# Performance work log

Measured on AMD Instinct MI355X. Metric: run time of the kernel, lower is better.

## Reference

```python
import jax, jax.numpy as jnp
import numpy as np

N, E = 50000, 800000
H, C = 4, 32          # heads, per-head channels
IN_DIM = 128
NEG_SLOPE = 0.2


def gat_conv(x, edge_index, W, a_src, a_dst, b):
    """PyG-style GATConv: Wx, per-edge leaky-relu logits, dst-segment softmax,
    scatter-weighted aggregation, concat heads, add bias. Self-loops added."""
    n = x.shape[0]
    loops = jnp.arange(n, dtype=edge_index.dtype)
    src = jnp.concatenate([edge_index[0], loops])
    dst = jnp.concatenate([edge_index[1], loops])
    xw = (x @ W).reshape(n, H, C)                      # [N,H,C]
    alpha_src = jnp.sum(xw * a_src, axis=-1)           # [N,H]
    alpha_dst = jnp.sum(xw * a_dst, axis=-1)           # [N,H]
    e = jax.nn.leaky_relu(alpha_src[src] + alpha_dst[dst], NEG_SLOPE)  # [E+N,H]
    m = jax.ops.segment_max(e, dst, num_segments=n)    # stable softmax per dst
    e = jnp.exp(e - m[dst])
    denom = jax.ops.segment_sum(e, dst, num_segments=n)
    alpha = e / denom[dst]                             # [E+N,H]
    out = jax.ops.segment_sum(alpha[:, :, None] * xw[src], dst, num_segments=n)
    return out.reshape(n, H * C) + b


def setup_inputs() -> dict:
    key = jax.random.key(0)
    ks = jax.random.split(key, 12)
    HC = H * C
    x = jax.random.normal(ks[0], (N, IN_DIM), dtype=jnp.float32)
    edge_index = jax.random.randint(ks[1], (2, E), 0, N, dtype=jnp.int32)
    s0 = 1.0 / np.sqrt(IN_DIM)
    s1 = 1.0 / np.sqrt(HC)
    return {
        "x": x,
        "edge_index": edge_index,
        "W0": jax.random.normal(ks[2], (IN_DIM, HC), dtype=jnp.float32) * s0,
        "a_src0": jax.random.normal(ks[3], (H, C), dtype=jnp.float32) * s1,
        "a_dst0": jax.random.normal(ks[4], (H, C), dtype=jnp.float32) * s1,
        "b0": jnp.zeros((HC,), dtype=jnp.float32),
        "W1": jax.random.normal(ks[5], (HC, HC), dtype=jnp.float32) * s1,
        "a_src1": jax.random.normal(ks[6], (H, C), dtype=jnp.float32) * s1,
        "a_dst1": jax.random.normal(ks[7], (H, C), dtype=jnp.float32) * s1,
        "b1": jnp.zeros((HC,), dtype=jnp.float32),
        "Wr": jax.random.normal(ks[8], (HC, 1), dtype=jnp.float32) * s1,
        "br": jnp.zeros((1,), dtype=jnp.float32),
    }


def reference(x, edge_index, W0, a_src0, a_dst0, b0, W1, a_src1, a_dst1, b1, Wr, br):
    h = jax.nn.elu(gat_conv(x, edge_index, W0, a_src0, a_dst0, b0))
    # F.dropout(training=False) -> identity (eval mode)
    h = jax.nn.elu(gat_conv(h, edge_index, W1, a_src1, a_dst1, b1))
    return h @ Wr + br
```

## Files before the change

### kernel.cpp

```cpp
#include <hip/hip_runtime.h>
#include <hip/hip_bf16.h>
#include <hip/hip_fp16.h>

#define DEV __device__ __forceinline__

DEV float lrelu(float x) { return x > 0.f ? x : 0.2f * x; }
DEV float elu(float x)   { return x > 0.f ? x : __expf(x) - 1.f; }

typedef _Float16 v2h __attribute__((ext_vector_type(2)));
DEV float fdot2(__half2 a, __half2 b, float c) {
    union { __half2 h; v2h v; } ua, ub;
    ua.h = a; ub.h = b;
    return __builtin_amdgcn_fdot2(ua.v, ub.v, c, false);
}

#define CAP 64

__global__ __launch_bounds__(256, 8)
void gemm0_scatter(const float* __restrict__ X, const float* __restrict__ W,
                   const float* __restrict__ a_src, const float* __restrict__ a_dst,
                   __half2* __restrict__ xw2, float* __restrict__ asrc,
                   float* __restrict__ adst, int n, int gblk,
                   const int* __restrict__ ei, int* __restrict__ deg,
                   int* __restrict__ col2, int E, int sblk) {
    if ((int)blockIdx.x >= gblk) {
        int stride = sblk * 256;
        for (int e = ((int)blockIdx.x - gblk) * 256 + (int)threadIdx.x; e < E;
             e += stride) {
            int s = ei[e], d = ei[E + e];
            int pos = atomicAdd(&deg[d], 1);
            if (pos < CAP) col2[d * CAP + pos] = s;
        }
        return;
    }
    __shared__ __half2 Xs2[16][68];
    __shared__ __half2 Ws2[16][132];
    int t = threadIdx.x;
    int n0 = (int)blockIdx.x * 64;
    int rg = t >> 4;
    int cg = t & 15;
    int q0 = cg * 8 + ((cg >= 8) ? 4 : 0);

    float acc[4][8];
#pragma unroll
    for (int r = 0; r < 4; ++r)
#pragma unroll
        for (int c = 0; c < 8; ++c) acc[r][c] = 0.f;

    float4 px[2], pw[4];
    auto load_x = [&](int k0, float4* p) {
#pragma unroll
        for (int it = 0; it < 2; ++it) {
            int idx = t + it * 256;
            int row = idx >> 3, kq = idx & 7;
            int gr = n0 + row;
            p[it] = (gr < n) ? *(const float4*)&X[(size_t)gr * 128 + k0 + kq * 4]
                             : make_float4(0.f, 0.f, 0.f, 0.f);
        }
    };
    auto load_w = [&](int k0, float4* p) {
#pragma unroll
        for (int it = 0; it < 2; ++it) {
            int idx = t + it * 256;
            int k2 = idx >> 5, cq = idx & 31;
            p[2 * it]     = *(const float4*)&W[(size_t)(k0 + 2 * k2) * 128 + cq * 4];
            p[2 * it + 1] = *(const float4*)&W[(size_t)(k0 + 2 * k2 + 1) * 128 + cq * 4];
        }
    };
    auto store_lds = [&](const float4* pX, const float4* pW) {
#pragma unroll
        for (int it = 0; it < 2; ++it) {
            int idx = t + it * 256;
            int row = idx >> 3, kq = idx & 7;
            Xs2[kq * 2 + 0][row] = __floats2half2_rn(pX[it].x, pX[it].y);
            Xs2[kq * 2 + 1][row] = __floats2half2_rn(pX[it].z, pX[it].w);
        }
#pragma unroll
        for (int it = 0; it < 2; ++it) {
            int idx = t + it * 256;
            int k2 = idx >> 5, cq = idx & 31;
            const float4 w0 = pW[2 * it], w1 = pW[2 * it + 1];
            union { __half2 h[4]; float4 f; } u;
            u.h[0] = __floats2half2_rn(w0.x, w1.x);
            u.h[1] = __floats2half2_rn(w0.y, w1.y);
            u.h[2] = __floats2half2_rn(w0.z, w1.z);
            u.h[3] = __floats2half2_rn(w0.w, w1.w);
            *(float4*)&Ws2[k2][cq * 4 + ((cq >= 16) ? 4 : 0)] = u.f;
        }
    };

    load_x(0, px);
    load_w(0, pw);
    for (int c4 = 0; c4 < 4; ++c4) {
        store_lds(px, pw);
        __syncthreads();
        if (c4 < 3) { load_x((c4 + 1) * 32, px); load_w((c4 + 1) * 32, pw); }
#pragma unroll 4
        for (int k2 = 0; k2 < 16; ++k2) {
            union { float4 f; __half2 h[4]; } ux, uw0, uw1;
            ux.f  = *(const float4*)&Xs2[k2][rg * 4];
            uw0.f = *(const float4*)&Ws2[k2][q0];
            uw1.f = *(const float4*)&Ws2[k2][q0 + 4];
            __half2 wr[8] = {uw0.h[0], uw0.h[1], uw0.h[2], uw0.h[3],
                             uw1.h[0], uw1.h[1], uw1.h[2], uw1.h[3]};
#pragma unroll
            for (int r = 0; r < 4; ++r)
#pragma unroll
                for (int c = 0; c < 8; ++c)
                    acc[r][c] = fdot2(ux.h[r], wr[c], acc[r][c]);
        }
        __syncthreads();
    }

    int c0 = cg * 8;
    int h = cg >> 2;
    float as8[8], ad8[8];
#pragma unroll
    for (int c = 0; c < 8; ++c) { as8[c] = a_src[c0 + c]; ad8[c] = a_dst[c0 + c]; }
#pragma unroll
    for (int r = 0; r < 4; ++r) {
        int gr = n0 + rg * 4 + r;
        float s_ = 0.f, d_ = 0.f;
#pragma unroll
        for (int c = 0; c < 8; ++c) {
            s_ = fmaf(acc[r][c], as8[c], s_);
            d_ = fmaf(acc[r][c], ad8[c], d_);
        }
        s_ += __shfl_xor(s_, 1); s_ += __shfl_xor(s_, 2);
        d_ += __shfl_xor(d_, 1); d_ += __shfl_xor(d_, 2);
        if (gr < n) {
            __half2* rowp = &xw2[(size_t)gr * 64 + (c0 >> 1)];
            rowp[0] = __floats2half2_rn(acc[r][0], acc[r][1]);
            rowp[1] = __floats2half2_rn(acc[r][2], acc[r][3]);
            rowp[2] = __floats2half2_rn(acc[r][4], acc[r][5]);
            rowp[3] = __floats2half2_rn(acc[r][6], acc[r][7]);
            if ((t & 3) == 0) { asrc[gr * 4 + h] = s_; adst[gr * 4 + h] = d_; }
        }
    }
}

__global__ __launch_bounds__(512, 8)
void agg0_gemm1(const __half2* __restrict__ xw2a, const float* __restrict__ asrc0,
                const float* __restrict__ adst0, const int* __restrict__ col2,
                const int* __restrict__ deg, const float* __restrict__ bias,
                const float* __restrict__ W, const float* __restrict__ a_src,
                const float* __restrict__ a_dst, __half2* __restrict__ xw2b,
                float* __restrict__ asrc1, float* __restrict__ adst1, int n) {
    __shared__ __half2 Xh2[64][66];
    __shared__ __half2 Ws2[16][132];
    int t = threadIdx.x;
    int n0 = (int)blockIdx.x * 64;
    int l = t & 63;
    int q = t >> 6;

    float4 pw[2];
    auto load_w = [&](int k0) {
        int k2 = t >> 5, cq = t & 31;
        pw[0] = *(const float4*)&W[(size_t)(k0 + 2 * k2) * 128 + cq * 4];
        pw[1] = *(const float4*)&W[(size_t)(k0 + 2 * k2 + 1) * 128 + cq * 4];
    };
    auto store_w = [&]() {
        int k2 = t >> 5, cq = t & 31;
        union { __half2 h[4]; float4 f; } u;
        u.h[0] = __floats2half2_rn(pw[0].x, pw[1].x);
        u.h[1] = __floats2half2_rn(pw[0].y, pw[1].y);
        u.h[2] = __floats2half2_rn(pw[0].z, pw[1].z);
        u.h[3] = __floats2half2_rn(pw[0].w, pw[1].w);
        *(float4*)&Ws2[k2][cq * 4 + ((cq >= 16) ? 4 : 0)] = u.f;
    };
    load_w(0);

    {
        int h4 = l & 3;
        int jj = l >> 2;
        int hA = l >> 4;
        for (int it = 0; it < 8; ++it) {
            int i = __builtin_amdgcn_readfirstlane(n0 + q * 8 + it);
            float rx = 0.f, ry = 0.f;
            if (i < n) {
                int beg = i * CAP;
                int dcount = deg[i]; if (dcount > CAP) dcount = CAP;
                int end = beg + dcount;
                float ad = adst0[i * 4 + h4];
                float wsum = __expf(lrelu(asrc0[i * 4 + h4] + ad));
                float wselfA = __shfl(wsum, hA);
                float2 row_i = __half22float2(xw2a[(size_t)i * 64 + l]);
                float2 a0 = make_float2(wselfA * row_i.x, wselfA * row_i.y);
                float2 a1 = make_float2(0.f, 0.f);
                float2 a2 = make_float2(0.f, 0.f);
                float2 a3 = make_float2(0.f, 0.f);
                int ce = beg;
                for (; ce + 16 <= end; ce += 16) {
                    int s = col2[ce + jj];
                    float wv = __expf(lrelu(asrc0[s * 4 + h4] + ad));
                    float sv = wv;
                    sv += __shfl_xor(sv, 4);
                    sv += __shfl_xor(sv, 8);
                    sv += __shfl_xor(sv, 16);
                    sv += __shfl_xor(sv, 32);
                    wsum += sv;
#pragma unroll
                    for (int j = 0; j < 16; j += 4) {
                        int s0 = col2[ce + j + 0];
                        int s1 = col2[ce + j + 1];
                        int s2 = col2[ce + j + 2];
                        int s3 = col2[ce + j + 3];
                        float g0 = __shfl(wv, (j + 0) * 4 + hA);
                        float g1 = __shfl(wv, (j + 1) * 4 + hA);
                        float g2 = __shfl(wv, (j + 2) * 4 + hA);
                        float g3 = __shfl(wv, (j + 3) * 4 + hA);
                        float2 v0 = __half22float2(xw2a[(size_t)s0 * 64 + l]);
                        float2 v1 = __half22float2(xw2a[(size_t)s1 * 64 + l]);
                        float2 v2 = __half22float2(xw2a[(size_t)s2 * 64 + l]);
                        float2 v3 = __half22float2(xw2a[(size_t)s3 * 64 + l]);
                        a0.x = fmaf(g0, v0.x, a0.x); a0.y = fmaf(g0, v0.y, a0.y);
                        a1.x = fmaf(g1, v1.x, a1.x); a1.y = fmaf(g1, v1.y, a1.y);
                        a2.x = fmaf(g2, v2.x, a2.x); a2.y = fmaf(g2, v2.y, a2.y);
                        a3.x = fmaf(g3, v3.x, a3.x); a3.y = fmaf(g3, v3.y, a3.y);
                    }
                }
                if (ce < end) {
                    int nc = end - ce;
                    float wv = 0.f;
                    if (jj < nc) {
                        int s = col2[ce + jj];
                        wv = __expf(lrelu(asrc0[s * 4 + h4] + ad));
                    }
                    float sv = wv;
                    sv += __shfl_xor(sv, 4);
                    sv += __shfl_xor(sv, 8);
                    sv += __shfl_xor(sv, 16);
                    sv += __shfl_xor(sv, 32);
                    wsum += sv;
#pragma unroll
                    for (int j = 0; j < 16; ++j) {
                        if (j >= nc) break;
                        int sj = col2[ce + j];
                        float wg = __shfl(wv, j * 4 + hA);
                        float2 v = __half22float2(xw2a[(size_t)sj * 64 + l]);
                        a0.x = fmaf(wg, v.x, a0.x);
                        a0.y = fmaf(wg, v.y, a0.y);
                    }
                }
                a0.x += (a1.x + a2.x) + a3.x;
                a0.y += (a1.y + a2.y) + a3.y;
                float wsA = __shfl(wsum, hA);
                float inv = 1.f / wsA;
                float2 bv = *(const float2*)&bias[2 * l];
                rx = elu(a0.x * inv + bv.x);
                ry = elu(a0.y * inv + bv.y);
            }
            int row = q * 8 + it;
            Xh2[l][row] = __floats2half2_rn(rx, ry);
        }
    }
    __syncthreads();

    int rg = t >> 4;
    int cg = t & 15;
    int q0 = cg * 8 + ((cg >= 8) ? 4 : 0);
    float acc[2][8];
#pragma unroll
    for (int r = 0; r < 2; ++r)
#pragma unroll
        for (int c = 0; c < 8; ++c) acc[r][c] = 0.f;

    for (int c4 = 0; c4 < 4; ++c4) {
        store_w();
        __syncthreads();
        if (c4 < 3) load_w((c4 + 1) * 32);
        int kb2 = c4 * 16;
#pragma unroll 4
        for (int k = 0; k < 16; ++k) {
            __half2 xv0 = Xh2[kb2 + k][rg * 2];
            __half2 xv1 = Xh2[kb2 + k][rg * 2 + 1];
            union { float4 f; __half2 h[4]; } uw0, uw1;
            uw0.f = *(const float4*)&Ws2[k][q0];
            uw1.f = *(const float4*)&Ws2[k][q0 + 4];
            __half2 wr[8] = {uw0.h[0], uw0.h[1], uw0.h[2], uw0.h[3],
                             uw1.h[0], uw1.h[1], uw1.h[2], uw1.h[3]};
#pragma unroll
            for (int c = 0; c < 8; ++c) {
                acc[0][c] = fdot2(xv0, wr[c], acc[0][c]);
                acc[1][c] = fdot2(xv1, wr[c], acc[1][c]);
            }
        }
        __syncthreads();
    }

    int c0 = cg * 8;
    int h = cg >> 2;
    float as8[8], ad8[8];
#pragma unroll
    for (int c = 0; c < 8; ++c) { as8[c] = a_src[c0 + c]; ad8[c] = a_dst[c0 + c]; }
#pragma unroll
    for (int r = 0; r < 2; ++r) {
        int gr = n0 + rg * 2 + r;
        float s_ = 0.f, d_ = 0.f;
#pragma unroll
        for (int c = 0; c < 8; ++c) {
            s_ = fmaf(acc[r][c], as8[c], s_);
            d_ = fmaf(acc[r][c], ad8[c], d_);
        }
        s_ += __shfl_xor(s_, 1); s_ += __shfl_xor(s_, 2);
        d_ += __shfl_xor(d_, 1); d_ += __shfl_xor(d_, 2);
        if (gr < n) {
            __half2* rowp = &xw2b[(size_t)gr * 64 + (c0 >> 1)];
            rowp[0] = __floats2half2_rn(acc[r][0], acc[r][1]);
            rowp[1] = __floats2half2_rn(acc[r][2], acc[r][3]);
            rowp[2] = __floats2half2_rn(acc[r][4], acc[r][5]);
            rowp[3] = __floats2half2_rn(acc[r][6], acc[r][7]);
            if ((t & 3) == 0) { asrc1[gr * 4 + h] = s_; adst1[gr * 4 + h] = d_; }
        }
    }
}

__global__ __launch_bounds__(256, 8)
void aggregate_v7(const __half2* __restrict__ xw2, const float* __restrict__ asrc,
                  const float* __restrict__ adst, const int* __restrict__ col2,
                  const int* __restrict__ deg, const float* __restrict__ bias,
                  float* __restrict__ out1, const float* __restrict__ Wr,
                  const float* __restrict__ br, int n) {
    int l = threadIdx.x & 63;
    int i = __builtin_amdgcn_readfirstlane((blockIdx.x * 256 + threadIdx.x) >> 6);
    if (i >= n) return;
    int h4 = l & 3;
    int jj = l >> 2;
    int hA = l >> 4;
    int beg = i * CAP;
    int dcount = deg[i]; if (dcount > CAP) dcount = CAP;
    int end = beg + dcount;
    float ad = adst[i * 4 + h4];
    float wsum = __expf(lrelu(asrc[i * 4 + h4] + ad));
    float wselfA = __shfl(wsum, hA);
    float2 row_i = __half22float2(xw2[(size_t)i * 64 + l]);
    float2 a0 = make_float2(wselfA * row_i.x, wselfA * row_i.y);
    float2 a1 = make_float2(0.f, 0.f);
    float2 a2 = make_float2(0.f, 0.f);
    float2 a3 = make_float2(0.f, 0.f);

    int ce = beg;
    for (; ce + 16 <= end; ce += 16) {
        int s = col2[ce + jj];
        float wv = __expf(lrelu(asrc[s * 4 + h4] + ad));
        float sv = wv;
        sv += __shfl_xor(sv, 4);
        sv += __shfl_xor(sv, 8);
        sv += __shfl_xor(sv, 16);
        sv += __shfl_xor(sv, 32);
        wsum += sv;
#pragma unroll
        for (int j = 0; j < 16; j += 4) {
            int s0 = col2[ce + j + 0];
            int s1 = col2[ce + j + 1];
            int s2 = col2[ce + j + 2];
            int s3 = col2[ce + j + 3];
            float g0 = __shfl(wv, (j + 0) * 4 + hA);
            float g1 = __shfl(wv, (j + 1) * 4 + hA);
            float g2 = __shfl(wv, (j + 2) * 4 + hA);
            float g3 = __shfl(wv, (j + 3) * 4 + hA);
            float2 v0 = __half22float2(xw2[(size_t)s0 * 64 + l]);
            float2 v1 = __half22float2(xw2[(size_t)s1 * 64 + l]);
            float2 v2 = __half22float2(xw2[(size_t)s2 * 64 + l]);
            float2 v3 = __half22float2(xw2[(size_t)s3 * 64 + l]);
            a0.x = fmaf(g0, v0.x, a0.x); a0.y = fmaf(g0, v0.y, a0.y);
            a1.x = fmaf(g1, v1.x, a1.x); a1.y = fmaf(g1, v1.y, a1.y);
            a2.x = fmaf(g2, v2.x, a2.x); a2.y = fmaf(g2, v2.y, a2.y);
            a3.x = fmaf(g3, v3.x, a3.x); a3.y = fmaf(g3, v3.y, a3.y);
        }
    }
    if (ce < end) {
        int nc = end - ce;
        float wv = 0.f;
        if (jj < nc) {
            int s = col2[ce + jj];
            wv = __expf(lrelu(asrc[s * 4 + h4] + ad));
        }
        float sv = wv;
        sv += __shfl_xor(sv, 4);
        sv += __shfl_xor(sv, 8);
        sv += __shfl_xor(sv, 16);
        sv += __shfl_xor(sv, 32);
        wsum += sv;
#pragma unroll
        for (int j = 0; j < 16; ++j) {
            if (j >= nc) break;
            int sj = col2[ce + j];
            float wg = __shfl(wv, j * 4 + hA);
            float2 v = __half22float2(xw2[(size_t)sj * 64 + l]);
            a0.x = fmaf(wg, v.x, a0.x);
            a0.y = fmaf(wg, v.y, a0.y);
        }
    }
    a0.x += (a1.x + a2.x) + a3.x;
    a0.y += (a1.y + a2.y) + a3.y;
    float wsA = __shfl(wsum, hA);
    float inv = 1.f / wsA;
    float2 bv = *(const float2*)&bias[2 * l];
    float rx = elu(a0.x * inv + bv.x);
    float ry = elu(a0.y * inv + bv.y);
    float v = rx * Wr[2 * l] + ry * Wr[2 * l + 1];
#pragma unroll
    for (int off = 32; off > 0; off >>= 1) v += __shfl_xor(v, off);
    if (l == 0) out1[i] = v + br[0];
}

extern "C" void kernel_launch(void* const* d_in, const int* in_sizes, int n_in,
                              void* d_out, int out_size, void* d_ws, size_t ws_size,
                              hipStream_t stream) {
    const float* x   = (const float*)d_in[0];
    const int*   ei  = (const int*)d_in[1];
    const float* W0  = (const float*)d_in[2];
    const float* as0 = (const float*)d_in[3];
    const float* ad0 = (const float*)d_in[4];
    const float* b0  = (const float*)d_in[5];
    const float* W1  = (const float*)d_in[6];
    const float* as1 = (const float*)d_in[7];
    const float* ad1 = (const float*)d_in[8];
    const float* b1  = (const float*)d_in[9];
    const float* Wr  = (const float*)d_in[10];
    const float* br  = (const float*)d_in[11];
    float* out = (float*)d_out;

    const int N = in_sizes[0] / 128;
    const int E = in_sizes[1] / 2;

    char* w = (char*)d_ws;
    size_t off = 0;
    auto alloc = [&](size_t bytes) -> void* {
        void* p = w + off;
        off += (bytes + 255) & ~size_t(255);
        return p;
    };
    __half2* xw2a  = (__half2*)alloc((size_t)N * 64 * 4);
    __half2* xw2b  = (__half2*)alloc((size_t)N * 64 * 4);
    float* asrc0   = (float*)alloc((size_t)N * 4 * 4);
    float* adst0   = (float*)alloc((size_t)N * 4 * 4);
    float* asrc1   = (float*)alloc((size_t)N * 4 * 4);
    float* adst1   = (float*)alloc((size_t)N * 4 * 4);
    int*   deg     = (int*)alloc((size_t)N * 4);
    int*   col2    = (int*)alloc((size_t)N * CAP * 4);

    hipMemsetAsync(deg, 0, (size_t)N * 4, stream);

    const int gblk = (N + 63) / 64;
    const int sblk = 768;
    const int ablk = (N + 3) / 4;
    gemm0_scatter<<<gblk + sblk, 256, 0, stream>>>(x, W0, as0, ad0, xw2a, asrc0,
                                                   adst0, N, gblk, ei, deg, col2,
                                                   E, sblk);
    agg0_gemm1<<<gblk, 512, 0, stream>>>(xw2a, asrc0, adst0, col2, deg, b0,
                                         W1, as1, ad1, xw2b, asrc1, adst1, N);
    aggregate_v7<<<ablk, 256, 0, stream>>>(xw2b, asrc1, adst1, col2, deg, b1,
                                           out, Wr, br, N);
}
```

Baseline: 281.2 us.

## Gather neighbor rows with 16-byte loads, four edges per wave in parallel

Adds a shared agg_wide helper in which each wave splits into four 16-lane groups. Each group processes a different neighbor per step and loads 8 halfs per lane with one float4, and the four partial accumulators are combined with cross-group shuffles at the end. Both aggregation kernels now use it, which replaces many 4-byte gathers with wider loads and drops the repeated per-lane col2 reads in favour of shuffles. It also lowers the launch-bounds occupancy hint for agg0_gemm1 to allow more registers, and doubles the number of scatter blocks. The risks are higher register pressure and extra shuffle reductions.

Measured after the change: 356.5 us. +26.8%, slower.

```diff
diff --git a/kernel.cpp b/kernel.cpp
--- a/kernel.cpp
+++ b/kernel.cpp
@@ -15,6 +15,109 @@
 }
 
 #define CAP 64
+
+DEV void agg_wide(int i, const __half* xwb, const float* __restrict__ asrc,
+                  const float* __restrict__ adst, const int* __restrict__ col2,
+                  const int* __restrict__ deg, const float* __restrict__ bias,
+                  int l, float* r) {
+    int h4 = l & 3;
+    int jj = l >> 2;
+    int g  = l >> 4;
+    int u  = l & 15;
+    int hh = u >> 2;
+    int beg = i * CAP;
+    int dc = deg[i]; if (dc > CAP) dc = CAP;
+    int end = beg + dc;
+    float ad = adst[i * 4 + h4];
+    float wself = __expf(lrelu(asrc[i * 4 + h4] + ad));
+    float wsum = wself;
+    float wselfA = __shfl(wself, hh);
+    float acc[8];
+    {
+        float4 raw = make_float4(0.f, 0.f, 0.f, 0.f);
+        if (g == 0) raw = *(const float4*)&xwb[(size_t)i * 128 + u * 8];
+        const __half2* hp = (const __half2*)&raw;
+#pragma unroll
+        for (int m = 0; m < 4; ++m) {
+            float2 f = __half22float2(hp[m]);
+            acc[2 * m]     = wselfA * f.x;
+            acc[2 * m + 1] = wselfA * f.y;
+        }
+    }
+    int ce = beg;
+    for (; ce + 16 <= end; ce += 16) {
+        int s = col2[ce + jj];
+        float wv = __expf(lrelu(asrc[s * 4 + h4] + ad));
+        float sv = wv;
+        sv += __shfl_xor(sv, 4);
+        sv += __shfl_xor(sv, 8);
+        sv += __shfl_xor(sv, 16);
+        sv += __shfl_xor(sv, 32);
+        wsum += sv;
+#pragma unroll
+        for (int p = 0; p < 4; ++p) {
+            int j = p * 4 + g;
+            int sj = __shfl(s, j * 4);
+            float wg = __shfl(wv, j * 4 + hh);
+            float4 raw = *(const float4*)&xwb[(size_t)sj * 128 + u * 8];
+            const __half2* hp = (const __half2*)&raw;
+#pragma unroll
+            for (int m = 0; m < 4; ++m) {
+                float2 f = __half22float2(hp[m]);
+                acc[2 * m]     = fmaf(wg, f.x, acc[2 * m]);
+                acc[2 * m + 1] = fmaf(wg, f.y, acc[2 * m + 1]);
+            }
+        }
+    }
+    if (ce < end) {
+        int nc = end - ce;
+        float wv = 0.f;
+        int s = 0;
+        if (jj < nc) {
+            s = col2[ce + jj];
+            wv = __expf(lrelu(asrc[s * 4 + h4] + ad));
+        }
+        float sv = wv;
+        sv += __shfl_xor(sv, 4);
+        sv += __shfl_xor(sv, 8);
+        sv += __shfl_xor(sv, 16);
+        sv += __shfl_xor(sv, 32);
+        wsum += sv;
+#pragma unroll
+        for (int p = 0; p < 4; ++p) {
+            int j = p * 4 + g;
+            int sj = __shfl(s, j * 4);
+            float wg = __shfl(wv, j * 4 + hh);
+            if (j < nc) {
+                float4 raw = *(const float4*)&xwb[(size_t)sj * 128 + u * 8];
+                const __half2* hp = (const __half2*)&raw;
+#pragma unroll
+                for (int m = 0; m < 4; ++m) {
+                    float2 f = __half22float2(hp[m]);
+                    acc[2 * m]     = fmaf(wg, f.x, acc[2 * m]);
+                    acc[2 * m + 1] = fmaf(wg, f.y, acc[2 * m + 1]);
+                }
+            }
+        }
+    }
+#pragma unroll
+    for (int c = 0; c < 8; ++c) {
+        acc[c] += __shfl_xor(acc[c], 16);
+        acc[c] += __shfl_xor(acc[c], 32);
+    }
+    float wsA = __shfl(wsum, hh);
+    float inv = 1.f / wsA;
+    float4 b0 = *(const float4*)&bias[u * 8];
+    float4 b1 = *(const float4*)&bias[u * 8 + 4];
+    r[0] = elu(acc[0] * inv + b0.x);
+    r[1] = elu(acc[1] * inv + b0.y);
+    r[2] = elu(acc[2] * inv + b0.z);
+    r[3] = elu(acc[3] * inv + b0.w);
+    r[4] = elu(acc[4] * inv + b1.x);
+    r[5] = elu(acc[5] * inv + b1.y);
+    r[6] = elu(acc[6] * inv + b1.z);
+    r[7] = elu(acc[7] * inv + b1.w);
+}
 
 __global__ __launch_bounds__(256, 8)
 void gemm0_scatter(const float* __restrict__ X, const float* __restrict__ W,
@@ -139,7 +242,7 @@
     }
 }
 
-__global__ __launch_bounds__(512, 8)
+__global__ __launch_bounds__(512, 6)
 void agg0_gemm1(const __half2* __restrict__ xw2a, const float* __restrict__ asrc0,
                 const float* __restrict__ adst0, const int* __restrict__ col2,
                 const int* __restrict__ deg, const float* __restrict__ bias,
@@ -171,87 +274,18 @@
     load_w(0);
 
     {
-        int h4 = l & 3;
-        int jj = l >> 2;
-        int hA = l >> 4;
         for (int it = 0; it < 8; ++it) {
             int i = __builtin_amdgcn_readfirstlane(n0 + q * 8 + it);
-            float rx = 0.f, ry = 0.f;
-            if (i < n) {
-                int beg = i * CAP;
-                int dcount = deg[i]; if (dcount > CAP) dcount = CAP;
-                int end = beg + dcount;
-                float ad = adst0[i * 4 + h4];
-                float wsum = __expf(lrelu(asrc0[i * 4 + h4] + ad));
-                float wselfA = __shfl(wsum, hA);
-                float2 row_i = __half22float2(xw2a[(size_t)i * 64 + l]);
-                float2 a0 = make_float2(wselfA * row_i.x, wselfA * row_i.y);
-                float2 a1 = make_float2(0.f, 0.f);
-                float2 a2 = make_float2(0.f, 0.f);
-                float2 a3 = make_float2(0.f, 0.f);
-                int ce = beg;
-                for (; ce + 16 <= end; ce += 16) {
-                    int s = col2[ce + jj];
-                    float wv = __expf(lrelu(asrc0[s * 4 + h4] + ad));
-                    float sv = wv;
-                    sv += __shfl_xor(sv, 4);
-                    sv += __shfl_xor(sv, 8);
-                    sv += __shfl_xor(sv, 16);
-                    sv += __shfl_xor(sv, 32);
-                    wsum += sv;
-#pragma unroll
-                    for (int j = 0; j < 16; j += 4) {
-                        int s0 = col2[ce + j + 0];
-                        int s1 = col2[ce + j + 1];
-                        int s2 = col2[ce + j + 2];
-                        int s3 = col2[ce + j + 3];
-                        float g0 = __shfl(wv, (j + 0) * 4 + hA);
-                        float g1 = __shfl(wv, (j + 1) * 4 + hA);
-                        float g2 = __shfl(wv, (j + 2) * 4 + hA);
-                        float g3 = __shfl(wv, (j + 3) * 4 + hA);
-                        float2 v0 = __half22float2(xw2a[(size_t)s0 * 64 + l]);
-                        float2 v1 = __half22float2(xw2a[(size_t)s1 * 64 + l]);
-                        float2 v2 = __half22float2(xw2a[(size_t)s2 * 64 + l]);
-                        float2 v3 = __half22float2(xw2a[(size_t)s3 * 64 + l]);
-                        a0.x = fmaf(g0, v0.x, a0.x); a0.y = fmaf(g0, v0.y, a0.y);
-                        a1.x = fmaf(g1, v1.x, a1.x); a1.y = fmaf(g1, v1.y, a1.y);
-                        a2.x = fmaf(g2, v2.x, a2.x); a2.y = fmaf(g2, v2.y, a2.y);
-                        a3.x = fmaf(g3, v3.x, a3.x); a3.y = fmaf(g3, v3.y, a3.y);
-                    }
-                }
-                if (ce < end) {
-                    int nc = end - ce;
-                    float wv = 0.f;
-                    if (jj < nc) {
-                        int s = col2[ce + jj];
-                        wv = __expf(lrelu(asrc0[s * 4 + h4] + ad));
-                    }
-                    float sv = wv;
-                    sv += __shfl_xor(sv, 4);
-                    sv += __shfl_xor(sv, 8);
-                    sv += __shfl_xor(sv, 16);
-                    sv += __shfl_xor(sv, 32);
-                    wsum += sv;
-#pragma unroll
-                    for (int j = 0; j < 16; ++j) {
-                        if (j >= nc) break;
-                        int sj = col2[ce + j];
-                        float wg = __shfl(wv, j * 4 + hA);
-                        float2 v = __half22float2(xw2a[(size_t)sj * 64 + l]);
-                        a0.x = fmaf(wg, v.x, a0.x);
-                        a0.y = fmaf(wg, v.y, a0.y);
-                    }
-                }
-                a0.x += (a1.x + a2.x) + a3.x;
-                a0.y += (a1.y + a2.y) + a3.y;
-                float wsA = __shfl(wsum, hA);
-                float inv = 1.f / wsA;
-                float2 bv = *(const float2*)&bias[2 * l];
-                rx = elu(a0.x * inv + bv.x);
-                ry = elu(a0.y * inv + bv.y);
+            float r[8] = {0.f, 0.f, 0.f, 0.f, 0.f, 0.f, 0.f, 0.f};
+            if (i < n)
+                agg_wide(i, (const __half*)xw2a, asrc0, adst0, col2, deg, bias, l, r);
+            int row = q * 8 + it;
+            if ((l >> 4) == 0) {
+                int u = l & 15;
+#pragma unroll
+                for (int m = 0; m < 4; ++m)
+                    Xh2[u * 4 + m][row] = __floats2half2_rn(r[2 * m], r[2 * m + 1]);
             }
-            int row = q * 8 + it;
-            Xh2[l][row] = __floats2half2_rn(rx, ry);
         }
     }
     __syncthreads();
@@ -316,92 +350,25 @@
 }
 
 __global__ __launch_bounds__(256, 8)
-void aggregate_v7(const __half2* __restrict__ xw2, const float* __restrict__ asrc,
-                  const float* __restrict__ adst, const int* __restrict__ col2,
-                  const int* __restrict__ deg, const float* __restrict__ bias,
-                  float* __restrict__ out1, const float* __restrict__ Wr,
-                  const float* __restrict__ br, int n) {
+void aggregate_head(const __half2* __restrict__ xw2, const float* __restrict__ asrc,
+                    const float* __restrict__ adst, const int* __restrict__ col2,
+                    const int* __restrict__ deg, const float* __restrict__ bias,
+                    float* __restrict__ out1, const float* __restrict__ Wr,
+                    const float* __restrict__ br, int n) {
     int l = threadIdx.x & 63;
     int i = __builtin_amdgcn_readfirstlane((blockIdx.x * 256 + threadIdx.x) >> 6);
     if (i >= n) return;
-    int h4 = l & 3;
-    int jj = l >> 2;
-    int hA = l >> 4;
-    int beg = i * CAP;
-    int dcount = deg[i]; if (dcount > CAP) dcount = CAP;
-    int end = beg + dcount;
-    float ad = adst[i * 4 + h4];
-    float wsum = __expf(lrelu(asrc[i * 4 + h4] + ad));
-    float wselfA = __shfl(wsum, hA);
-    float2 row_i = __half22float2(xw2[(size_t)i * 64 + l]);
-    float2 a0 = make_float2(wselfA * row_i.x, wselfA * row_i.y);
-    float2 a1 = make_float2(0.f, 0.f);
-    float2 a2 = make_float2(0.f, 0.f);
-    float2 a3 = make_float2(0.f, 0.f);
-
-    int ce = beg;
-    for (; ce + 16 <= end; ce += 16) {
-        int s = col2[ce + jj];
-        float wv = __expf(lrelu(asrc[s * 4 + h4] + ad));
-        float sv = wv;
-        sv += __shfl_xor(sv, 4);
-        sv += __shfl_xor(sv, 8);
-        sv += __shfl_xor(sv, 16);
-        sv += __shfl_xor(sv, 32);
-        wsum += sv;
-#pragma unroll
-        for (int j = 0; j < 16; j += 4) {
-            int s0 = col2[ce + j + 0];
-            int s1 = col2[ce + j + 1];
-            int s2 = col2[ce + j + 2];
-            int s3 = col2[ce + j + 3];
-            float g0 = __shfl(wv, (j + 0) * 4 + hA);
-            float g1 = __shfl(wv, (j + 1) * 4 + hA);
-            float g2 = __shfl(wv, (j + 2) * 4 + hA);
-            float g3 = __shfl(wv, (j + 3) * 4 + hA);
-            float2 v0 = __half22float2(xw2[(size_t)s0 * 64 + l]);
-            float2 v1 = __half22float2(xw2[(size_t)s1 * 64 + l]);
-            float2 v2 = __half22float2(xw2[(size_t)s2 * 64 + l]);
-            float2 v3 = __half22float2(xw2[(size_t)s3 * 64 + l]);
-            a0.x = fmaf(g0, v0.x, a0.x); a0.y = fmaf(g0, v0.y, a0.y);
-            a1.x = fmaf(g1, v1.x, a1.x); a1.y = fmaf(g1, v1.y, a1.y);
-            a2.x = fmaf(g2, v2.x, a2.x); a2.y = fmaf(g2, v2.y, a2.y);
-            a3.x = fmaf(g3, v3.x, a3.x); a3.y = fmaf(g3, v3.y, a3.y);
-        }
-    }
-    if (ce < end) {
-        int nc = end - ce;
-        float wv = 0.f;
-        if (jj < nc) {
-            int s = col2[ce + jj];
-            wv = __expf(lrelu(asrc[s * 4 + h4] + ad));
-        }
-        float sv = wv;
-        sv += __shfl_xor(sv, 4);
-        sv += __shfl_xor(sv, 8);
-        sv += __shfl_xor(sv, 16);
-        sv += __shfl_xor(sv, 32);
-        wsum += sv;
-#pragma unroll
-        for (int j = 0; j < 16; ++j) {
-            if (j >= nc) break;
-            int sj = col2[ce + j];
-            float wg = __shfl(wv, j * 4 + hA);
-            float2 v = __half22float2(xw2[(size_t)sj * 64 + l]);
-            a0.x = fmaf(wg, v.x, a0.x);
-            a0.y = fmaf(wg, v.y, a0.y);
-        }
-    }
-    a0.x += (a1.x + a2.x) + a3.x;
-    a0.y += (a1.y + a2.y) + a3.y;
-    float wsA = __shfl(wsum, hA);
-    float inv = 1.f / wsA;
-    float2 bv = *(const float2*)&bias[2 * l];
-    float rx = elu(a0.x * inv + bv.x);
-    float ry = elu(a0.y * inv + bv.y);
-    float v = rx * Wr[2 * l] + ry * Wr[2 * l + 1];
-#pragma unroll
-    for (int off = 32; off > 0; off >>= 1) v += __shfl_xor(v, off);
+    float r[8];
+    agg_wide(i, (const __half*)xw2, asrc, adst, col2, deg, bias, l, r);
+    int u = l & 15;
+    float4 w0 = *(const float4*)&Wr[u * 8];
+    float4 w1 = *(const float4*)&Wr[u * 8 + 4];
+    float v = r[0] * w0.x + r[1] * w0.y + r[2] * w0.z + r[3] * w0.w
+            + r[4] * w1.x + r[5] * w1.y + r[6] * w1.z + r[7] * w1.w;
+    v += __shfl_xor(v, 1);
+    v += __shfl_xor(v, 2);
+    v += __shfl_xor(v, 4);
+    v += __shfl_xor(v, 8);
     if (l == 0) out1[i] = v + br[0];
 }
 
@@ -444,13 +411,13 @@
     hipMemsetAsync(deg, 0, (size_t)N * 4, stream);
 
     const int gblk = (N + 63) / 64;
-    const int sblk = 768;
+    const int sblk = 1536;
     const int ablk = (N + 3) / 4;
     gemm0_scatter<<<gblk + sblk, 256, 0, stream>>>(x, W0, as0, ad0, xw2a, asrc0,
                                                    adst0, N, gblk, ei, deg, col2,
                                                    E, sblk);
     agg0_gemm1<<<gblk, 512, 0, stream>>>(xw2a, asrc0, adst0, col2, deg, b0,
                                          W1, as1, ad1, xw2b, asrc1, adst1, N);
-    aggregate_v7<<<ablk, 256, 0, stream>>>(xw2b, asrc1, adst1, col2, deg, b1,
-                                           out, Wr, br, N);
-}
+    aggregate_head<<<ablk, 256, 0, stream>>>(xw2b, asrc1, adst1, col2, deg, b1,
+                                             out, Wr, br, N);
+}
```
